# Kernel optimization log

Measured on AMD Instinct MI355X. Metric: run time of the kernel, lower is better.

The kernel has to match this reference:

```python
import jax, jax.numpy as jnp
import numpy as np

NB, B, C, L = 4, 16, 256, 4096
BN_EPS = 1e-5


def setup_inputs() -> dict:
    key = jax.random.key(0)
    ks = jax.random.split(key, 10)
    s = 0.02
    return {
        "x": jax.random.normal(ks[0], (NB, B, C, L), jnp.float32),
        "Wq": jax.random.normal(ks[1], (NB, C, C), jnp.float32) * s,
        "bq": jax.random.normal(ks[2], (NB, C), jnp.float32) * s,
        "Wk": jax.random.normal(ks[3], (NB, C, C), jnp.float32) * s,
        "bk": jax.random.normal(ks[4], (NB, C), jnp.float32) * s,
        "Wv": jax.random.normal(ks[5], (NB, C, C), jnp.float32) * s,
        "bv": jax.random.normal(ks[6], (NB, C), jnp.float32) * s,
        "Wo": jax.random.normal(ks[7], (NB, C, C), jnp.float32) * s,
        "bo": jax.random.normal(ks[8], (NB, C), jnp.float32) * s,
        "gamma": jnp.ones((NB, C), jnp.float32),
        "beta": jnp.zeros((NB, C), jnp.float32),
        "edge_w": jnp.ones((NB, NB), jnp.float32),
        "branch_imp": jnp.ones((NB,), jnp.float32),
    }


def _proj(W, b, x):
    # 1x1 Conv1d == per-branch channel mixing: [nb,o,c] x [nb,B,c,L] -> [nb,B,o,L]
    return jnp.einsum('noc,nbcl->nbol', W, x) + b[:, None, :, None]


def reference(x, Wq, bq, Wk, bk, Wv, bv, Wo, bo, gamma, beta, edge_w, branch_imp):
    feat_dim = x.shape[2]
    scale = jnp.sqrt(jnp.asarray(feat_dim, x.dtype))
    q = _proj(Wq, bq, x)
    k = _proj(Wk, bk, x)
    v = _proj(Wv, bv, x)
    # descriptors: [nb, B, C, 2] = (mean over L, max over L)
    qd = jnp.stack([q.mean(axis=-1), q.max(axis=-1)], axis=-1)
    kd = jnp.stack([k.mean(axis=-1), k.max(axis=-1)], axis=-1)
    # mean over 2x2 bmm entries == (sum_p qd)(sum_q kd) summed over C, / 4
    scores = jnp.einsum('ibcp,jbcq->ijb', qd, kd) / (4.0 * scale)
    scores = scores * edge_w[:, :, None]
    attn = jax.nn.softmax(scores, axis=1) * jax.nn.softmax(branch_imp)[None, :, None]
    # weighted aggregation over source branches j
    agg = jnp.einsum('ijb,jbcl->ibcl', attn, v)
    out = _proj(Wo, bo, agg)
    # BatchNorm1d (training-mode batch statistics over B and L per channel, per branch)
    mean = out.mean(axis=(1, 3), keepdims=True)
    var = out.var(axis=(1, 3), keepdims=True)
    bn = (out - mean) * jax.lax.rsqrt(var + BN_EPS)
    bn = bn * gamma[:, None, :, None] + beta[:, None, :, None]
    return jax.nn.relu(bn) + x
```

## Files before the change

### kernel.cpp

```cpp
#include <hip/hip_runtime.h>
#include <stdint.h>
#include <stddef.h>

#define NBR 4
#define BSZ 16
#define CHN 256
#define LEN 4096
#define NB_B 64
#define BL   65536
#define BN_EPS 1e-5f
#define W_EL (NBR*CHN*CHN)

typedef unsigned short ushortT;
typedef unsigned short ushort4_t __attribute__((ext_vector_type(4)));
typedef unsigned short ushort8_t __attribute__((ext_vector_type(8)));
typedef short bf16x8 __attribute__((ext_vector_type(8)));
typedef float f32x4 __attribute__((ext_vector_type(4)));

__device__ __forceinline__ float bf2f(ushortT u) {
    return __uint_as_float(((unsigned)u) << 16);
}
__device__ __forceinline__ ushortT f2bf(float f) {
    unsigned b = __float_as_uint(f);
    return (ushortT)((b + 0x7FFFu + ((b >> 16) & 1u)) >> 16);
}
__device__ __forceinline__ unsigned encf(float f) {
    unsigned b = __float_as_uint(f);
    return (b & 0x80000000u) ? ~b : (b | 0x80000000u);
}
__device__ __forceinline__ float decf(unsigned u) {
    unsigned b = (u & 0x80000000u) ? (u ^ 0x80000000u) : ~u;
    return __uint_as_float(b);
}

__device__ __forceinline__ int swzX(int row, int cb) {
    return row * 512 + (cb ^ ((row & 7) << 4) ^ (((row >> 3) & 3) << 7));
}
__device__ __forceinline__ int swzW(int row, int cb) {
    return row * 128 + (cb ^ ((row & 7) << 4));
}

__device__ __forceinline__ void stage_w_load(const ushortT* Wb, int obase, int kb, int tid,
                                             ushort8_t wreg[4])
{
    const int r = tid >> 1;
    const int h = tid & 1;
    const ushortT* wp = Wb + (size_t)(obase + r) * CHN + kb + h * 32;
#pragma unroll
    for (int i = 0; i < 4; ++i) wreg[i] = *(const ushort8_t*)(wp + i * 8);
}
__device__ __forceinline__ void stage_w_write(ushortT* sW, int tid, const ushort8_t wreg[4])
{
    const int r = tid >> 1;
    const int h = tid & 1;
#pragma unroll
    for (int i = 0; i < 4; ++i)
        *(ushort8_t*)((char*)sW + swzW(r, h * 64 + i * 16)) = wreg[i];
}

template <bool SWAP>
__device__ __forceinline__ void mfma_chunk(const ushortT* sX, const ushortT* sW,
                                           f32x4 acc[4][4], int wr, int wc, int lane, int kb)
{
    const int am = wr * 64 + (lane & 15);
    const int bo = wc * 64 + (lane & 15);
    const int kg = (lane >> 4) * 16;
#pragma unroll
    for (int s = 0; s < 2; ++s) {
        bf16x8 a[4], b[4];
#pragma unroll
        for (int mf = 0; mf < 4; ++mf)
            a[mf] = *(const bf16x8*)((const char*)sX + swzX(am + mf * 16, kb * 2 + s * 64 + kg));
#pragma unroll
        for (int nf = 0; nf < 4; ++nf)
            b[nf] = *(const bf16x8*)((const char*)sW + swzW(bo + nf * 16, s * 64 + kg));
#pragma unroll
        for (int mf = 0; mf < 4; ++mf)
#pragma unroll
            for (int nf = 0; nf < 4; ++nf) {
                if (!SWAP)
                    acc[mf][nf] = __builtin_amdgcn_mfma_f32_16x16x32_bf16(a[mf], b[nf], acc[mf][nf], 0, 0, 0);
                else
                    acc[nf][mf] = __builtin_amdgcn_mfma_f32_16x16x32_bf16(b[nf], a[mf], acc[nf][mf], 0, 0, 0);
            }
    }
}

__global__ __launch_bounds__(256, 2)
void qkv_kernel(const float* __restrict__ x, const ushortT* __restrict__ Wbf,
                const float* __restrict__ bv,
                float* __restrict__ qsum, unsigned* __restrict__ qmax,
                float* __restrict__ ksum, unsigned* __restrict__ kmax,
                ushortT* __restrict__ vT)
{
    __shared__ ushortT sX[128 * 256];
    __shared__ ushortT sW[128 * 64];
    const int tid = threadIdx.x;
    const int lane = tid & 63;
    const int wv = tid >> 6;
    const int wr = wv >> 1, wc = wv & 1;
    const int lbase = blockIdx.x * 128;
    const int z = blockIdx.y;
    const int n = z >> 4;

    ushort8_t wreg[4];
    stage_w_load(Wbf + (size_t)n * CHN * CHN, 0, 0, tid, wreg);

    {
        float* raw = (float*)sW;
        const int tq = tid >> 5;
        const int tl = tid & 31;
        const int l  = tid & 127;
        const int h  = tid >> 7;
        const float* xz = x + (size_t)z * CHN * LEN + lbase;
        float4 v4[4];
#pragma unroll
        for (int q = 0; q < 4; ++q)
            v4[q] = *(const float4*)(xz + (size_t)(q * 8 + tq) * LEN + tl * 4);
        for (int cc = 0; cc < 8; ++cc) {
            __syncthreads();
#pragma unroll
            for (int q = 0; q < 4; ++q)
                *(float4*)(raw + (q * 8 + tq) * 128 + tl * 4) = v4[q];
            if (cc < 7) {
#pragma unroll
                for (int q = 0; q < 4; ++q)
                    v4[q] = *(const float4*)(xz + (size_t)((cc + 1) * 32 + q * 8 + tq) * LEN + tl * 4);
            }
            __syncthreads();
#pragma unroll
            for (int p = 0; p < 2; ++p) {
                int oct = h * 2 + p;
                ushort8_t u8;
#pragma unroll
                for (int i = 0; i < 8; ++i) u8[i] = f2bf(raw[(oct * 8 + i) * 128 + l]);
                *(ushort8_t*)((char*)sX + swzX(l, (cc * 32 + oct * 8) * 2)) = u8;
            }
        }
    }

    for (int w = 0; w < 3; ++w) {
        for (int ot = 0; ot < 2; ++ot) {
            const int obase = ot * 128;
            f32x4 acc[4][4];
            const f32x4 z4 = {0.f, 0.f, 0.f, 0.f};
#pragma unroll
            for (int mf = 0; mf < 4; ++mf)
#pragma unroll
                for (int nf = 0; nf < 4; ++nf) acc[mf][nf] = z4;

#pragma unroll
            for (int kb = 0; kb < 4; ++kb) {
                __syncthreads();
                stage_w_write(sW, tid, wreg);
                int cidx = (w * 2 + ot) * 4 + kb + 1;
                if (cidx < 24) {
                    int nw = cidx >> 3, not_ = (cidx >> 2) & 1, nkb = cidx & 3;
                    stage_w_load(Wbf + ((size_t)nw * NBR + n) * CHN * CHN,
                                 not_ * 128, nkb * 64, tid, wreg);
                }
                __syncthreads();
                if (w < 2) mfma_chunk<false>(sX, sW, acc, wr, wc, lane, kb * 64);
                else       mfma_chunk<true >(sX, sW, acc, wr, wc, lane, kb * 64);
            }

            if (w < 2) {
                float* rs = (w == 0) ? qsum : ksum;
                unsigned* rm = (w == 0) ? qmax : kmax;
#pragma unroll
                for (int nf = 0; nf < 4; ++nf) {
                    float s = 0.f, m = -3.4e38f;
#pragma unroll
                    for (int mf = 0; mf < 4; ++mf)
#pragma unroll
                        for (int r = 0; r < 4; ++r) {
                            float v = acc[mf][nf][r];
                            s += v; m = fmaxf(m, v);
                        }
                    s += __shfl_xor(s, 16); s += __shfl_xor(s, 32);
                    m = fmaxf(m, __shfl_xor(m, 16)); m = fmaxf(m, __shfl_xor(m, 32));
                    if (lane < 16) {
                        int o = obase + wc * 64 + nf * 16 + lane;
                        atomicAdd(&rs[z * CHN + o], s);
                        atomicMax(&rm[z * CHN + o], encf(m));
                    }
                }
            } else {
#pragma unroll
                for (int nf = 0; nf < 4; ++nf) {
                    int o0 = obase + wc * 64 + nf * 16 + ((lane >> 4) << 2);
                    float b4[4];
#pragma unroll
                    for (int r = 0; r < 4; ++r) b4[r] = bv[n * CHN + o0 + r];
#pragma unroll
                    for (int mf = 0; mf < 4; ++mf) {
                        int l = lbase + wr * 64 + mf * 16 + (lane & 15);
                        ushort4_t u;
#pragma unroll
                        for (int r = 0; r < 4; ++r) u[r] = f2bf(acc[nf][mf][r] + b4[r]);
                        *(ushort4_t*)(vT + ((size_t)z * LEN + l) * CHN + o0) = u;
                    }
                }
            }
        }
    }
}

__global__ __launch_bounds__(256, 2)
void ogemm_kernel(const ushortT* __restrict__ vT, const ushortT* __restrict__ Wbo,
                  const float* __restrict__ attn, const float* __restrict__ bo_,
                  float* __restrict__ bnsum, float* __restrict__ bnss,
                  ushortT* __restrict__ outpre)
{
    __shared__ ushortT sX[128 * 256];
    __shared__ ushortT sW[128 * 64];
    const int tid = threadIdx.x;
    const int lane = tid & 63;
    const int wv = tid >> 6;
    const int wr = wv >> 1, wc = wv & 1;
    const int lbase = blockIdx.x * 128;
    const int z = blockIdx.y;
    const int n = z >> 4;
    const int b_ = z & 15;
    const ushortT* Wb = Wbo + (size_t)n * CHN * CHN;

    ushort8_t wreg[4];
    stage_w_load(Wb, 0, 0, tid, wreg);

    float aj[4];
#pragma unroll
    for (int j = 0; j < 4; ++j) aj[j] = attn[(n * 4 + j) * BSZ + b_];

#pragma unroll 4
    for (int u = 0; u < 16; ++u) {
        int g = u * 256 + tid;
        int l = g >> 5;
        int cg = g & 31;
        size_t boff = ((size_t)lbase + l) * CHN + cg * 8;
        float acc8[8];
#pragma unroll
        for (int e = 0; e < 8; ++e) acc8[e] = 0.f;
#pragma unroll
        for (int j = 0; j < 4; ++j) {
            ushort8_t r8 = *(const ushort8_t*)(vT + (size_t)(j * BSZ + b_) * LEN * CHN + boff);
#pragma unroll
            for (int e = 0; e < 8; ++e) acc8[e] += aj[j] * bf2f(r8[e]);
        }
        ushort8_t o8;
#pragma unroll
        for (int e = 0; e < 8; ++e) o8[e] = f2bf(acc8[e]);
        *(ushort8_t*)((char*)sX + swzX(l, cg * 16)) = o8;
    }

    for (int ot = 0; ot < 2; ++ot) {
        const int obase = ot * 128;
        f32x4 acc[4][4];
        const f32x4 z4 = {0.f, 0.f, 0.f, 0.f};
#pragma unroll
        for (int mf = 0; mf < 4; ++mf)
#pragma unroll
            for (int nf = 0; nf < 4; ++nf) acc[mf][nf] = z4;

#pragma unroll
        for (int kb = 0; kb < 4; ++kb) {
            __syncthreads();
            stage_w_write(sW, tid, wreg);
            int cidx = ot * 4 + kb + 1;
            if (cidx < 8) {
                int not_ = (cidx >> 2) & 1, nkb = cidx & 3;
                stage_w_load(Wb, not_ * 128, nkb * 64, tid, wreg);
            }
            __syncthreads();
            mfma_chunk<false>(sX, sW, acc, wr, wc, lane, kb * 64);
        }

#pragma unroll
        for (int nf = 0; nf < 4; ++nf) {
            int o = obase + wc * 64 + nf * 16 + (lane & 15);
            float bb = bo_[n * CHN + o];
            float s = 0.f, q2 = 0.f;
#pragma unroll
            for (int mf = 0; mf < 4; ++mf) {
                int l = lbase + wr * 64 + mf * 16 + ((lane >> 4) << 2);
                ushort4_t u;
#pragma unroll
                for (int r = 0; r < 4; ++r) {
                    float v = acc[mf][nf][r] + bb;
                    u[r] = f2bf(v);
                    s += v; q2 += v * v;
                }
                *(ushort4_t*)(outpre + (size_t)(z * CHN + o) * LEN + l) = u;
            }
            s += __shfl_xor(s, 16); s += __shfl_xor(s, 32);
            q2 += __shfl_xor(q2, 16); q2 += __shfl_xor(q2, 32);
            if (lane < 16) {
                atomicAdd(&bnsum[n * CHN + o], s);
                atomicAdd(&bnss[n * CHN + o], q2);
            }
        }
    }
}

__global__ void wcvt_kernel(const float* __restrict__ Wq, const float* __restrict__ Wk,
                            const float* __restrict__ Wv, const float* __restrict__ Wo,
                            ushortT* __restrict__ Wbf)
{
    int t = blockIdx.x * 256 + threadIdx.x;
    const int per = W_EL / 4;
    if (t < 4 * per) {
        const float* srcs[4] = {Wq, Wk, Wv, Wo};
        int w = t / per;
        int r = t - w * per;
        float4 f = *(const float4*)(srcs[w] + (size_t)r * 4);
        ushort4_t u = {f2bf(f.x), f2bf(f.y), f2bf(f.z), f2bf(f.w)};
        *(ushort4_t*)(Wbf + (size_t)w * W_EL + (size_t)r * 4) = u;
    }
}

__global__ void attn_kernel(const float* __restrict__ qsum, const unsigned* __restrict__ qmax,
                            const float* __restrict__ ksum, const unsigned* __restrict__ kmax,
                            const float* __restrict__ bq, const float* __restrict__ bk,
                            const float* __restrict__ edge, const float* __restrict__ bimp,
                            float* __restrict__ attn)
{
    __shared__ float sc[NBR][NBR][BSZ];
    int tid = threadIdx.x;
    int i = tid >> 6, j = (tid >> 4) & 3, b = tid & 15;
    float s = 0.f;
    const float invL = 1.0f / (float)LEN;
    for (int c = 0; c < CHN; ++c) {
        int qi = (i * BSZ + b) * CHN + c;
        int ki = (j * BSZ + b) * CHN + c;
        float sq = qsum[qi] * invL + decf(qmax[qi]) + 2.f * bq[i * CHN + c];
        float sk = ksum[ki] * invL + decf(kmax[ki]) + 2.f * bk[j * CHN + c];
        s += sq * sk;
    }
    sc[i][j][b] = s * edge[i * 4 + j] * (1.0f / 64.0f);
    __syncthreads();
    if (tid < 64) {
        int ii = tid >> 4, bb = tid & 15;
        float m = -3.4e38f;
        for (int jj = 0; jj < 4; ++jj) m = fmaxf(m, sc[ii][jj][bb]);
        float e[4]; float sum = 0.f;
        for (int jj = 0; jj < 4; ++jj) { e[jj] = __expf(sc[ii][jj][bb] - m); sum += e[jj]; }
        float bm = fmaxf(fmaxf(bimp[0], bimp[1]), fmaxf(bimp[2], bimp[3]));
        float be[4]; float bs = 0.f;
        for (int jj = 0; jj < 4; ++jj) { be[jj] = __expf(bimp[jj] - bm); bs += be[jj]; }
        for (int jj = 0; jj < 4; ++jj)
            attn[(ii * 4 + jj) * BSZ + bb] = (e[jj] / sum) * (be[jj] / bs);
    }
}

__global__ void bnfin_kernel(const float* __restrict__ bnsum, const float* __restrict__ bnss,
                             const float* __restrict__ gamma, const float* __restrict__ beta,
                             float* __restrict__ scl, float* __restrict__ shf)
{
    int t = blockIdx.x * blockDim.x + threadIdx.x;
    if (t < NBR * CHN) {
        const float inv = 1.0f / (float)BL;
        float mean = bnsum[t] * inv;
        float var = bnss[t] * inv - mean * mean;
        float rs = rsqrtf(var + BN_EPS);
        float s = gamma[t] * rs;
        scl[t] = s;
        shf[t] = beta[t] - mean * s;
    }
}

__global__ __launch_bounds__(256)
void final_kernel(const ushortT* __restrict__ outpre, const float* __restrict__ x,
                  const float* __restrict__ scl, const float* __restrict__ shf,
                  float* __restrict__ out)
{
    const long long U = (long long)NB_B * CHN * (LEN / 8);
    for (long long u = (long long)blockIdx.x * blockDim.x + threadIdx.x; u < U;
         u += (long long)gridDim.x * blockDim.x) {
        int l0 = (int)(u & 511) * 8;
        int c  = (int)(u >> 9) & 255;
        int zz = (int)(u >> 17);
        int n  = zz >> 4;
        size_t base = ((size_t)zz * CHN + c) * LEN + l0;
        ushort8_t op = *(const ushort8_t*)(outpre + base);
        float4 x0 = *(const float4*)(x + base);
        float4 x1 = *(const float4*)(x + base + 4);
        float sc = scl[n * CHN + c];
        float sh = shf[n * CHN + c];
        float xr[8] = {x0.x, x0.y, x0.z, x0.w, x1.x, x1.y, x1.z, x1.w};
        float res[8];
#pragma unroll
        for (int e = 0; e < 8; ++e) {
            float bn = bf2f(op[e]) * sc + sh;
            res[e] = fmaxf(bn, 0.f) + xr[e];
        }
        float4 o0 = {res[0], res[1], res[2], res[3]};
        float4 o1 = {res[4], res[5], res[6], res[7]};
        *(float4*)(out + base) = o0;
        *(float4*)(out + base + 4) = o1;
    }
}

extern "C" void kernel_launch(void* const* d_in, const int* in_sizes, int n_in,
                              void* d_out, int out_size, void* d_ws, size_t ws_size,
                              hipStream_t stream)
{
    const float* x     = (const float*)d_in[0];
    const float* Wq    = (const float*)d_in[1];
    const float* bq    = (const float*)d_in[2];
    const float* Wk    = (const float*)d_in[3];
    const float* bk    = (const float*)d_in[4];
    const float* Wv    = (const float*)d_in[5];
    const float* bv    = (const float*)d_in[6];
    const float* Wo    = (const float*)d_in[7];
    const float* bo    = (const float*)d_in[8];
    const float* gamma = (const float*)d_in[9];
    const float* beta  = (const float*)d_in[10];
    const float* edge  = (const float*)d_in[11];
    const float* bimp  = (const float*)d_in[12];

    char* ws = (char*)d_ws;
    const size_t P_BYTES = (size_t)NBR * BSZ * CHN * LEN * 2;
    ushortT* outpre = (ushortT*)ws;
    size_t off = P_BYTES;
    float*    qsum = (float*)(ws + off);    off += 65536;
    unsigned* qmax = (unsigned*)(ws + off); off += 65536;
    float*    ksum = (float*)(ws + off);    off += 65536;
    unsigned* kmax = (unsigned*)(ws + off); off += 65536;
    float*    attn = (float*)(ws + off);    off += 1024;
    float*    bnsum= (float*)(ws + off);    off += 4096;
    float*    bnss = (float*)(ws + off);    off += 4096;
    float*    scl  = (float*)(ws + off);    off += 4096;
    float*    shf  = (float*)(ws + off);    off += 4096;

    hipMemsetAsync(ws + P_BYTES, 0, off - P_BYTES, stream);

    ushortT* vT  = (ushortT*)d_out;
    ushortT* Wbf = (ushortT*)((char*)d_out + ((size_t)134217728));
    float*   outf = (float*)d_out;

    wcvt_kernel<<<(4 * W_EL / 4 + 255) / 256, 256, 0, stream>>>(Wq, Wk, Wv, Wo, Wbf);

    dim3 gq(LEN / 128, NB_B);
    qkv_kernel<<<gq, 256, 0, stream>>>(x, Wbf, bv, qsum, qmax, ksum, kmax, vT);
    attn_kernel<<<1, 256, 0, stream>>>(qsum, qmax, ksum, kmax, bq, bk, edge, bimp, attn);
    ogemm_kernel<<<gq, 256, 0, stream>>>(vT, Wbf + (size_t)3 * W_EL, attn, bo, bnsum, bnss, outpre);
    bnfin_kernel<<<4, 256, 0, stream>>>(bnsum, bnss, gamma, beta, scl, shf);
    final_kernel<<<8192, 256, 0, stream>>>(outpre, x, scl, shf, outf);
}
```

Before: 540.4 us.

## Load GEMM weight fragments directly from global memory instead of staging in LDS

Removes the shared-memory weight staging buffer and its per-k-block double sync in both the QKV and output GEMM kernels. MFMA B fragments are now read straight from global (L2-cached) bf16 weights. The x fp32-to-bf16 staging is simplified to direct strided global loads without an LDS transpose buffer, and the V projection computes both output halves back-to-back into two accumulator sets. This lowers LDS use and barrier count, which could raise occupancy. The cost is global-load latency exposed on the MFMA path, uncoalesced strided x reads, and higher register pressure from the doubled accumulators.

New measurement: 634.2 us. 17.4% more time.

```diff
diff --git a/kernel.cpp b/kernel.cpp
--- a/kernel.cpp
+++ b/kernel.cpp
@@ -36,44 +36,40 @@
 __device__ __forceinline__ int swzX(int row, int cb) {
     return row * 512 + (cb ^ ((row & 7) << 4) ^ (((row >> 3) & 3) << 7));
 }
-__device__ __forceinline__ int swzW(int row, int cb) {
-    return row * 128 + (cb ^ ((row & 7) << 4));
-}
-
-__device__ __forceinline__ void stage_w_load(const ushortT* Wb, int obase, int kb, int tid,
-                                             ushort8_t wreg[4])
-{
-    const int r = tid >> 1;
-    const int h = tid & 1;
-    const ushortT* wp = Wb + (size_t)(obase + r) * CHN + kb + h * 32;
-#pragma unroll
-    for (int i = 0; i < 4; ++i) wreg[i] = *(const ushort8_t*)(wp + i * 8);
-}
-__device__ __forceinline__ void stage_w_write(ushortT* sW, int tid, const ushort8_t wreg[4])
-{
-    const int r = tid >> 1;
-    const int h = tid & 1;
-#pragma unroll
-    for (int i = 0; i < 4; ++i)
-        *(ushort8_t*)((char*)sW + swzW(r, h * 64 + i * 16)) = wreg[i];
+
+__device__ __forceinline__ void stage_x_f32(const float* x, ushortT* sX, int z, int lbase, int tid)
+{
+    const int ls = tid & 127;
+    const int gh = tid >> 7;
+    const float* xp = x + (size_t)z * CHN * LEN + lbase + ls;
+#pragma unroll
+    for (int g = 0; g < 16; ++g) {
+        int c0 = (gh * 16 + g) * 8;
+        ushort8_t u;
+#pragma unroll
+        for (int i = 0; i < 8; ++i) u[i] = f2bf(xp[(size_t)(c0 + i) * LEN]);
+        *(ushort8_t*)((char*)sX + swzX(ls, c0 * 2)) = u;
+    }
 }
 
 template <bool SWAP>
-__device__ __forceinline__ void mfma_chunk(const ushortT* sX, const ushortT* sW,
-                                           f32x4 acc[4][4], int wr, int wc, int lane, int kb)
+__device__ __forceinline__ void mfma_chunk_g(const ushortT* sX, const ushortT* __restrict__ Wb,
+                                             int obase, f32x4 acc[4][4],
+                                             int wr, int wc, int lane, int kb)
 {
     const int am = wr * 64 + (lane & 15);
-    const int bo = wc * 64 + (lane & 15);
+    const int orow = obase + wc * 64 + (lane & 15);
     const int kg = (lane >> 4) * 16;
+    const int ke = (lane >> 4) * 8;
 #pragma unroll
     for (int s = 0; s < 2; ++s) {
         bf16x8 a[4], b[4];
 #pragma unroll
+        for (int nf = 0; nf < 4; ++nf)
+            b[nf] = *(const bf16x8*)(Wb + (size_t)(orow + nf * 16) * CHN + kb * 64 + s * 32 + ke);
+#pragma unroll
         for (int mf = 0; mf < 4; ++mf)
-            a[mf] = *(const bf16x8*)((const char*)sX + swzX(am + mf * 16, kb * 2 + s * 64 + kg));
-#pragma unroll
-        for (int nf = 0; nf < 4; ++nf)
-            b[nf] = *(const bf16x8*)((const char*)sW + swzW(bo + nf * 16, s * 64 + kg));
+            a[mf] = *(const bf16x8*)((const char*)sX + swzX(am + mf * 16, kb * 128 + s * 64 + kg));
 #pragma unroll
         for (int mf = 0; mf < 4; ++mf)
 #pragma unroll
@@ -94,7 +90,6 @@
                 ushortT* __restrict__ vT)
 {
     __shared__ ushortT sX[128 * 256];
-    __shared__ ushortT sW[128 * 64];
     const int tid = threadIdx.x;
     const int lane = tid & 63;
     const int wv = tid >> 6;
@@ -103,104 +98,83 @@
     const int z = blockIdx.y;
     const int n = z >> 4;
 
-    ushort8_t wreg[4];
-    stage_w_load(Wbf + (size_t)n * CHN * CHN, 0, 0, tid, wreg);
-
-    {
-        float* raw = (float*)sW;
-        const int tq = tid >> 5;
-        const int tl = tid & 31;
-        const int l  = tid & 127;
-        const int h  = tid >> 7;
-        const float* xz = x + (size_t)z * CHN * LEN + lbase;
-        float4 v4[4];
-#pragma unroll
-        for (int q = 0; q < 4; ++q)
-            v4[q] = *(const float4*)(xz + (size_t)(q * 8 + tq) * LEN + tl * 4);
-        for (int cc = 0; cc < 8; ++cc) {
-            __syncthreads();
-#pragma unroll
-            for (int q = 0; q < 4; ++q)
-                *(float4*)(raw + (q * 8 + tq) * 128 + tl * 4) = v4[q];
-            if (cc < 7) {
-#pragma unroll
-                for (int q = 0; q < 4; ++q)
-                    v4[q] = *(const float4*)(xz + (size_t)((cc + 1) * 32 + q * 8 + tq) * LEN + tl * 4);
-            }
-            __syncthreads();
-#pragma unroll
-            for (int p = 0; p < 2; ++p) {
-                int oct = h * 2 + p;
-                ushort8_t u8;
-#pragma unroll
-                for (int i = 0; i < 8; ++i) u8[i] = f2bf(raw[(oct * 8 + i) * 128 + l]);
-                *(ushort8_t*)((char*)sX + swzX(l, (cc * 32 + oct * 8) * 2)) = u8;
-            }
-        }
-    }
-
-    for (int w = 0; w < 3; ++w) {
+    stage_x_f32(x, sX, z, lbase, tid);
+    __syncthreads();
+
+    const f32x4 z4 = {0.f, 0.f, 0.f, 0.f};
+
+#pragma unroll
+    for (int w = 0; w < 2; ++w) {
+        const ushortT* Wb = Wbf + ((size_t)w * NBR + n) * CHN * CHN;
+        float* rs = (w == 0) ? qsum : ksum;
+        unsigned* rm = (w == 0) ? qmax : kmax;
         for (int ot = 0; ot < 2; ++ot) {
             const int obase = ot * 128;
             f32x4 acc[4][4];
-            const f32x4 z4 = {0.f, 0.f, 0.f, 0.f};
 #pragma unroll
             for (int mf = 0; mf < 4; ++mf)
 #pragma unroll
                 for (int nf = 0; nf < 4; ++nf) acc[mf][nf] = z4;
-
-#pragma unroll
-            for (int kb = 0; kb < 4; ++kb) {
-                __syncthreads();
-                stage_w_write(sW, tid, wreg);
-                int cidx = (w * 2 + ot) * 4 + kb + 1;
-                if (cidx < 24) {
-                    int nw = cidx >> 3, not_ = (cidx >> 2) & 1, nkb = cidx & 3;
-                    stage_w_load(Wbf + ((size_t)nw * NBR + n) * CHN * CHN,
-                                 not_ * 128, nkb * 64, tid, wreg);
+#pragma unroll
+            for (int kb = 0; kb < 4; ++kb)
+                mfma_chunk_g<false>(sX, Wb, obase, acc, wr, wc, lane, kb);
+
+#pragma unroll
+            for (int nf = 0; nf < 4; ++nf) {
+                float s = 0.f, m = -3.4e38f;
+#pragma unroll
+                for (int mf = 0; mf < 4; ++mf)
+#pragma unroll
+                    for (int r = 0; r < 4; ++r) {
+                        float v = acc[mf][nf][r];
+                        s += v; m = fmaxf(m, v);
+                    }
+                s += __shfl_xor(s, 16); s += __shfl_xor(s, 32);
+                m = fmaxf(m, __shfl_xor(m, 16)); m = fmaxf(m, __shfl_xor(m, 32));
+                if (lane < 16) {
+                    int o = obase + wc * 64 + nf * 16 + lane;
+                    atomicAdd(&rs[z * CHN + o], s);
+                    atomicMax(&rm[z * CHN + o], encf(m));
                 }
-                __syncthreads();
-                if (w < 2) mfma_chunk<false>(sX, sW, acc, wr, wc, lane, kb * 64);
-                else       mfma_chunk<true >(sX, sW, acc, wr, wc, lane, kb * 64);
-            }
-
-            if (w < 2) {
-                float* rs = (w == 0) ? qsum : ksum;
-                unsigned* rm = (w == 0) ? qmax : kmax;
-#pragma unroll
-                for (int nf = 0; nf < 4; ++nf) {
-                    float s = 0.f, m = -3.4e38f;
-#pragma unroll
-                    for (int mf = 0; mf < 4; ++mf)
-#pragma unroll
-                        for (int r = 0; r < 4; ++r) {
-                            float v = acc[mf][nf][r];
-                            s += v; m = fmaxf(m, v);
-                        }
-                    s += __shfl_xor(s, 16); s += __shfl_xor(s, 32);
-                    m = fmaxf(m, __shfl_xor(m, 16)); m = fmaxf(m, __shfl_xor(m, 32));
-                    if (lane < 16) {
-                        int o = obase + wc * 64 + nf * 16 + lane;
-                        atomicAdd(&rs[z * CHN + o], s);
-                        atomicMax(&rm[z * CHN + o], encf(m));
-                    }
+            }
+        }
+    }
+
+    {
+        const ushortT* Wb = Wbf + ((size_t)2 * NBR + n) * CHN * CHN;
+        f32x4 acc[4][4], acc2[4][4];
+#pragma unroll
+        for (int i = 0; i < 4; ++i)
+#pragma unroll
+            for (int j = 0; j < 4; ++j) { acc[i][j] = z4; acc2[i][j] = z4; }
+#pragma unroll
+        for (int kb = 0; kb < 4; ++kb)
+            mfma_chunk_g<true>(sX, Wb, 0, acc, wr, wc, lane, kb);
+#pragma unroll
+        for (int kb = 0; kb < 4; ++kb)
+            mfma_chunk_g<true>(sX, Wb, 128, acc2, wr, wc, lane, kb);
+
+#pragma unroll
+        for (int nf = 0; nf < 4; ++nf) {
+            const int c128 = wc * 64 + nf * 16 + ((lane >> 4) << 2);
+            float b0[4], b1[4];
+#pragma unroll
+            for (int r = 0; r < 4; ++r) {
+                b0[r] = bv[n * CHN + c128 + r];
+                b1[r] = bv[n * CHN + 128 + c128 + r];
+            }
+#pragma unroll
+            for (int mf = 0; mf < 4; ++mf) {
+                const int l = lbase + wr * 64 + mf * 16 + (lane & 15);
+                const size_t rowb = ((size_t)z * LEN + l) * CHN;
+                ushort4_t u0, u1;
+#pragma unroll
+                for (int r = 0; r < 4; ++r) {
+                    u0[r] = f2bf(acc[nf][mf][r] + b0[r]);
+                    u1[r] = f2bf(acc2[nf][mf][r] + b1[r]);
                 }
-            } else {
-#pragma unroll
-                for (int nf = 0; nf < 4; ++nf) {
-                    int o0 = obase + wc * 64 + nf * 16 + ((lane >> 4) << 2);
-                    float b4[4];
-#pragma unroll
-                    for (int r = 0; r < 4; ++r) b4[r] = bv[n * CHN + o0 + r];
-#pragma unroll
-                    for (int mf = 0; mf < 4; ++mf) {
-                        int l = lbase + wr * 64 + mf * 16 + (lane & 15);
-                        ushort4_t u;
-#pragma unroll
-                        for (int r = 0; r < 4; ++r) u[r] = f2bf(acc[nf][mf][r] + b4[r]);
-                        *(ushort4_t*)(vT + ((size_t)z * LEN + l) * CHN + o0) = u;
-                    }
-                }
+                *(ushort4_t*)(vT + rowb + c128) = u0;
+                *(ushort4_t*)(vT + rowb + 128 + c128) = u1;
             }
         }
     }
@@ -213,7 +187,6 @@
                   ushortT* __restrict__ outpre)
 {
     __shared__ ushortT sX[128 * 256];
-    __shared__ ushortT sW[128 * 64];
     const int tid = threadIdx.x;
     const int lane = tid & 63;
     const int wv = tid >> 6;
@@ -224,9 +197,6 @@
     const int b_ = z & 15;
     const ushortT* Wb = Wbo + (size_t)n * CHN * CHN;
 
-    ushort8_t wreg[4];
-    stage_w_load(Wb, 0, 0, tid, wreg);
-
     float aj[4];
 #pragma unroll
     for (int j = 0; j < 4; ++j) aj[j] = attn[(n * 4 + j) * BSZ + b_];
@@ -251,6 +221,7 @@
         for (int e = 0; e < 8; ++e) o8[e] = f2bf(acc8[e]);
         *(ushort8_t*)((char*)sX + swzX(l, cg * 16)) = o8;
     }
+    __syncthreads();
 
     for (int ot = 0; ot < 2; ++ot) {
         const int obase = ot * 128;
@@ -260,19 +231,9 @@
         for (int mf = 0; mf < 4; ++mf)
 #pragma unroll
             for (int nf = 0; nf < 4; ++nf) acc[mf][nf] = z4;
-
-#pragma unroll
-        for (int kb = 0; kb < 4; ++kb) {
-            __syncthreads();
-            stage_w_write(sW, tid, wreg);
-            int cidx = ot * 4 + kb + 1;
-            if (cidx < 8) {
-                int not_ = (cidx >> 2) & 1, nkb = cidx & 3;
-                stage_w_load(Wb, not_ * 128, nkb * 64, tid, wreg);
-            }
-            __syncthreads();
-            mfma_chunk<false>(sX, sW, acc, wr, wc, lane, kb * 64);
-        }
+#pragma unroll
+        for (int kb = 0; kb < 4; ++kb)
+            mfma_chunk_g<false>(sX, Wb, obase, acc, wr, wc, lane, kb);
 
 #pragma unroll
         for (int nf = 0; nf < 4; ++nf) {
```
